# Kernel tuning notes

Hardware: AMD Instinct MI355X
Metric: run time of the kernel (lower is better)

The kernel has to match this reference:

```python
import jax, jax.numpy as jnp
import numpy as np

B = 32768      # number of sets
N = 131072     # total elements
DIM = 128      # feature dim
HID = 64       # hidden dim
MAXP = 17      # max_n + 1 (one-hot positional dim / size-class count)


def _ln(x, g, b, eps=1e-5):
    m = jnp.mean(x, -1, keepdims=True)
    v = jnp.var(x, -1, keepdims=True)
    return (x - m) * jax.lax.rsqrt(v + eps) * g + b


def _mlp_ln(x, w1, b1, g, bt, w2, b2):
    return jnp.tanh(_ln(x @ w1 + b1, g, bt)) @ w2 + b2


def _mlp(x, w1, b1, w2, b2):
    return jnp.tanh(x @ w1 + b1) @ w2 + b2


def _lin_init(key, fan_in, fan_out):
    k1, k2 = jax.random.split(key)
    s = 1.0 / np.sqrt(fan_in)
    return (jax.random.uniform(k1, (fan_in, fan_out), jnp.float32, -s, s),
            jax.random.uniform(k2, (fan_out,), jnp.float32, -s, s))


def setup_inputs() -> dict:
    key = jax.random.key(0)
    ks = jax.random.split(key, 16)
    inp = {}
    inp['x'] = jax.random.normal(ks[0], (N, DIM), jnp.float32)
    inp['batch'] = jnp.sort(jax.random.randint(ks[1], (N,), 0, B)).astype(jnp.int64)
    # rank: Linear(dim, 1)
    inp['rank_w'], inp['rank_b'] = _lin_init(ks[2], DIM, 1)
    # enc_psi: dim -> 96 -> hid, LayerNorm
    inp['psi_w1'], inp['psi_b1'] = _lin_init(ks[3], DIM, 96)
    inp['psi_g'] = jnp.ones((96,), jnp.float32); inp['psi_bt'] = jnp.zeros((96,), jnp.float32)
    inp['psi_w2'], inp['psi_b2'] = _lin_init(ks[4], 96, HID)
    # encoder pos_encoder: 17 -> 40 -> hid, LayerNorm
    inp['pe_e_w1'], inp['pe_e_b1'] = _lin_init(ks[5], MAXP, 40)
    inp['pe_e_g'] = jnp.ones((40,), jnp.float32); inp['pe_e_bt'] = jnp.zeros((40,), jnp.float32)
    inp['pe_e_w2'], inp['pe_e_b2'] = _lin_init(ks[6], 40, HID)
    # enc_phi: (hid+17)=81 -> 72 -> hid, no LN
    inp['phi_w1'], inp['phi_b1'] = _lin_init(ks[7], HID + MAXP, 72)
    inp['phi_w2'], inp['phi_b2'] = _lin_init(ks[8], 72, HID)
    # size_pred: hid -> 40 -> 17, no LN
    inp['size_w1'], inp['size_b1'] = _lin_init(ks[9], HID, 40)
    inp['size_w2'], inp['size_b2'] = _lin_init(ks[10], 40, MAXP)
    # decoder pos_encoder: 17 -> 40 -> hid, LayerNorm
    inp['pe_d_w1'], inp['pe_d_b1'] = _lin_init(ks[11], MAXP, 40)
    inp['pe_d_g'] = jnp.ones((40,), jnp.float32); inp['pe_d_bt'] = jnp.zeros((40,), jnp.float32)
    inp['pe_d_w2'], inp['pe_d_b2'] = _lin_init(ks[12], 40, HID)
    # decoder: hid -> 96 -> dim, no LN
    inp['dec_w1'], inp['dec_b1'] = _lin_init(ks[13], HID, 96)
    inp['dec_w2'], inp['dec_b2'] = _lin_init(ks[14], 96, DIM)
    return inp


def reference(x, batch, rank_w, rank_b,
              psi_w1, psi_b1, psi_g, psi_bt, psi_w2, psi_b2,
              pe_e_w1, pe_e_b1, pe_e_g, pe_e_bt, pe_e_w2, pe_e_b2,
              phi_w1, phi_b1, phi_w2, phi_b2,
              size_w1, size_b1, size_w2, size_b2,
              pe_d_w1, pe_d_b1, pe_d_g, pe_d_bt, pe_d_w2, pe_d_b2,
              dec_w1, dec_b1, dec_w2, dec_b2):
    batch = batch.astype(jnp.int32)
    # ---- Encoder ----
    n = jax.ops.segment_sum(jnp.ones(N, jnp.int32), batch, num_segments=B)  # [B]
    seg_start = jnp.cumsum(n) - n                                           # ptr[:-1]
    mag = (x @ rank_w + rank_b).reshape(-1)                                 # rank scores
    idx = jnp.lexsort((mag, batch))  # per-segment sort (batch is grouped/sorted)
    xs = x[idx]                                                             # [N, DIM]
    keys = jnp.arange(N) - seg_start[batch]                                 # position in set
    pos = jax.nn.one_hot(keys, MAXP, dtype=x.dtype)                         # [N, MAXP]
    y1 = _mlp_ln(xs, psi_w1, psi_b1, psi_g, psi_bt, psi_w2, psi_b2) * \
         _mlp_ln(pos, pe_e_w1, pe_e_b1, pe_e_g, pe_e_bt, pe_e_w2, pe_e_b2)
    y2 = jax.ops.segment_sum(y1, batch, num_segments=B)                     # [B, HID]
    pos_n = jax.nn.one_hot(n, MAXP, dtype=x.dtype)
    z = _mlp(jnp.concatenate([y2, pos_n], -1), phi_w1, phi_b1, phi_w2, phi_b2)  # [B, HID]
    # ---- Decoder ----
    logits = _mlp(z, size_w1, size_b1, size_w2, size_b2)                    # [B, MAXP]
    n_dec = jnp.argmax(logits, -1)                                          # [B]
    pe = _mlp_ln(jnp.eye(MAXP, dtype=x.dtype),
                 pe_d_w1, pe_d_b1, pe_d_g, pe_d_bt, pe_d_w2, pe_d_b2)       # [MAXP, HID]
    zp = z[:, None, :] * pe[None, :, :]                                     # [B, MAXP, HID]
    xr = _mlp(zp, dec_w1, dec_b1, dec_w2, dec_b2)                           # [B, MAXP, DIM]
    mask = jnp.arange(MAXP)[None, :] < n_dec[:, None]                       # valid slots
    xr = jnp.where(mask[..., None], xr, 0.0)
    batchr = jnp.broadcast_to(jnp.arange(B)[:, None], (B, MAXP))
    return xr.reshape(B * MAXP, DIM), batchr.reshape(-1), mask.reshape(-1)
```

## Files before the change

### kernel.cpp

```cpp
#include <hip/hip_runtime.h>

#define NELEM 131072
#define BSETS 32768
#define DIM 128
#define HID 64
#define MAXP 17

typedef __attribute__((ext_vector_type(8))) short short8;
typedef __attribute__((ext_vector_type(4))) float f32x4;

__device__ __forceinline__ unsigned short f2bf(float f) {
  unsigned u = __float_as_uint(f);
  u += 0x7fff + ((u >> 16) & 1);
  return (unsigned short)(u >> 16);
}

__device__ __forceinline__ float fast_tanh(float x) {
  float t = __expf(2.0f * x);
  float r = __builtin_amdgcn_rcpf(t + 1.0f);
  return fmaf(-2.0f, r, 1.0f);
}

__device__ void pos_mlp40(int row, const float* w1, const float* b1, const float* g,
                          const float* bt, const float* w2, const float* b2, float* out) {
  float h[40];
  for (int j = 0; j < 40; ++j) h[j] = b1[j] + (row >= 0 ? w1[row * 40 + j] : 0.0f);
  float s = 0.f;
  for (int j = 0; j < 40; ++j) s += h[j];
  float mean = s * (1.0f / 40.0f);
  float v = 0.f;
  for (int j = 0; j < 40; ++j) { float d = h[j] - mean; v += d * d; }
  float rs = rsqrtf(v * (1.0f / 40.0f) + 1e-5f);
  float tb[40];
  for (int j = 0; j < 40; ++j) tb[j] = fast_tanh((h[j] - mean) * rs * g[j] + bt[j]);
  for (int o = 0; o < 64; ++o) {
    float a = b2[o];
    for (int j = 0; j < 40; ++j) a += tb[j] * w2[j * 64 + o];
    out[o] = a;
  }
}

__global__ __launch_bounds__(256) void k_init(
    const float* __restrict__ x, const int* __restrict__ batch,
    const float* __restrict__ rank_w, const float* __restrict__ rank_b,
    double* __restrict__ mag, int* __restrict__ start,
    const float* ew1, const float* eb1, const float* eg, const float* ebt,
    const float* ew2, const float* eb2,
    const float* dw1, const float* db1, const float* dg, const float* dbt,
    const float* dw2, const float* db2,
    float* enc_tab, float* dec_tab,
    const float* __restrict__ decw1, const float* __restrict__ decw2,
    unsigned short* __restrict__ w1s, unsigned short* __restrict__ w2s) {
  int blk = blockIdx.x;
  int t = threadIdx.x;
  if (blk < 1024) {
    int lane = t & 63;
    int w = t >> 6;
    float2 wv = ((const float2*)rank_w)[lane];
    double w0 = wv.x, w1 = wv.y;
    double rb = rank_b[0];
    int rowbase = (blk * 4 + w) * 32;
    for (int it = 0; it < 32; ++it) {
      int row = rowbase + it;
      float2 xv = ((const float2*)(x + (size_t)row * DIM))[lane];
      double acc = (double)xv.x * w0 + (double)xv.y * w1;
#pragma unroll
      for (int m = 1; m < 64; m <<= 1)
        acc += __shfl_xor(acc, m, 64);
      if (lane == 0) mag[row] = acc + rb;
    }
  } else if (blk < 1536) {
    int i = (blk - 1024) * 256 + t;
    int b = batch[i];
    if (i == 0) {
      for (int bb = 0; bb <= b; ++bb) start[bb] = 0;
    } else {
      int bp = batch[i - 1];
      for (int bb = bp + 1; bb <= b; ++bb) start[bb] = i;
    }
    if (i == NELEM - 1) {
      for (int bb = b + 1; bb <= BSETS; ++bb) start[bb] = NELEM;
    }
  } else if (blk == 1536) {
    if (t < 18) {
      float out[64];
      pos_mlp40(t < 17 ? t : -1, ew1, eb1, eg, ebt, ew2, eb2, out);
      for (int o = 0; o < 64; ++o) enc_tab[t * 64 + o] = out[o];
    } else if (t >= 32 && t < 49) {
      float out[64];
      pos_mlp40(t - 32, dw1, db1, dg, dbt, dw2, db2, out);
      for (int o = 0; o < 64; ++o) dec_tab[(t - 32) * 64 + o] = out[o];
    }
  } else {
    int idx = (blk - 1537) * 256 + t;
    if (idx < 6144) {
      int i = idx & 7, lane = (idx >> 3) & 63, rest = idx >> 9;
      int jt = rest % 6, s = rest / 6;
      int k = s * 32 + (lane >> 4) * 8 + i;
      int n = jt * 16 + (lane & 15);
      w1s[idx] = f2bf(decw1[k * 96 + n]);
    }
    int idx2 = idx - 6144;
    if (idx2 >= 0 && idx2 < 12288) {
      int i = idx2 & 7, lane = (idx2 >> 3) & 63, rest = idx2 >> 9;
      int jt = rest % 8, s = rest / 8;
      int k = s * 32 + (lane >> 4) * 8 + i;
      int n = jt * 16 + (lane & 15);
      w2s[idx2] = f2bf(decw2[k * 128 + n]);
    }
  }
}

__global__ __launch_bounds__(256) void k_encoder(
    const float* __restrict__ x, const int* __restrict__ batch,
    const double* __restrict__ mag, const int* __restrict__ start,
    const float* __restrict__ w1, const float* __restrict__ b1,
    const float* __restrict__ g, const float* __restrict__ bt,
    const float* __restrict__ w2, const float* __restrict__ b2,
    const float* __restrict__ enc_tab, float* __restrict__ y1) {
  __shared__ float sm[64 * 129];
  __shared__ float ps1[4][64];
  __shared__ float ps2[4][64];
  int t = threadIdx.x;
  int base = blockIdx.x * 64;
  const float4* xg = (const float4*)(x + (size_t)base * DIM);
#pragma unroll
  for (int v = 0; v < 8; ++v) {
    int f = t + 256 * v;
    float4 val = xg[f];
    int e = f >> 5, kq = (f & 31) * 4;
    float* xr = sm + e * 129 + kq;
    xr[0] = val.x; xr[1] = val.y; xr[2] = val.z; xr[3] = val.w;
  }
  int lane = t & 63;
  int w = __builtin_amdgcn_readfirstlane(t >> 6);
  int gi = base + lane;
  int bseg = batch[gi];
  int segs = start[bseg], sege = start[bseg + 1];
  double mi = mag[gi];
  int kk = 0;
  for (int j = segs; j < sege; ++j) {
    double mj = mag[j];
    kk += (mj < mi) || (mj == mi && j < gi);
  }
  __syncthreads();
  int j0 = w * 24;
  float acc[24];
#pragma unroll
  for (int jj = 0; jj < 24; ++jj) acc[jj] = b1[j0 + jj];
  for (int k = 0; k < DIM; ++k) {
    float xv = sm[lane * 129 + k];
#pragma unroll
    for (int jj = 0; jj < 24; ++jj) acc[jj] += xv * w1[k * 96 + j0 + jj];
  }
  float s1 = 0.f, s2 = 0.f;
#pragma unroll
  for (int jj = 0; jj < 24; ++jj) { s1 += acc[jj]; s2 += acc[jj] * acc[jj]; }
  ps1[w][lane] = s1; ps2[w][lane] = s2;
  __syncthreads();
  float S1 = ps1[0][lane] + ps1[1][lane] + ps1[2][lane] + ps1[3][lane];
  float S2 = ps2[0][lane] + ps2[1][lane] + ps2[2][lane] + ps2[3][lane];
  float mean = S1 * (1.0f / 96.0f);
  float var = S2 * (1.0f / 96.0f) - mean * mean;
  float rs = rsqrtf(var + 1e-5f);
#pragma unroll
  for (int jj = 0; jj < 24; ++jj) {
    float hv = (acc[jj] - mean) * rs * g[j0 + jj] + bt[j0 + jj];
    sm[lane * 97 + j0 + jj] = fast_tanh(hv);
  }
  __syncthreads();
  int o0 = w * 16;
  float acc2[16];
#pragma unroll
  for (int oo = 0; oo < 16; ++oo) acc2[oo] = b2[o0 + oo];
  for (int j = 0; j < 96; ++j) {
    float tv = sm[lane * 97 + j];
#pragma unroll
    for (int oo = 0; oo < 16; ++oo) acc2[oo] += tv * w2[j * 64 + o0 + oo];
  }
  int row = kk < MAXP ? kk : MAXP;
  int pos = segs + kk;
  const float* pe = enc_tab + row * 64;
#pragma unroll
  for (int oo = 0; oo < 16; ++oo) acc2[oo] *= pe[o0 + oo];
  float4* d4 = (float4*)(y1 + (size_t)pos * 64 + o0);
#pragma unroll
  for (int q = 0; q < 4; ++q)
    d4[q] = make_float4(acc2[4 * q], acc2[4 * q + 1], acc2[4 * q + 2], acc2[4 * q + 3]);
}

__global__ __launch_bounds__(256) void k_phi(const float* __restrict__ y1,
                                             const int* __restrict__ start,
                                             const float* __restrict__ w1, const float* __restrict__ b1,
                                             const float* __restrict__ w2, const float* __restrict__ b2,
                                             const float* __restrict__ sw1, const float* __restrict__ sb1,
                                             const float* __restrict__ sw2, const float* __restrict__ sb2,
                                             float* __restrict__ z, int* __restrict__ ndec) {
  __shared__ float yt[64][65];
  __shared__ float tt[64][73];
  __shared__ float zt[64][65];
  __shared__ float st[64][41];
  int t = threadIdx.x;
  int base = blockIdx.x * 64;
  {
    int s = t >> 2, c = t & 3;
    int sb = base + s;
    int ps = start[sb], pe = start[sb + 1];
    float acc[16];
#pragma unroll
    for (int i = 0; i < 16; ++i) acc[i] = 0.f;
    for (int p = ps; p < pe; ++p) {
      const float4* row = (const float4*)(y1 + (size_t)p * 64 + c * 16);
#pragma unroll
      for (int q = 0; q < 4; ++q) {
        float4 v = row[q];
        acc[4 * q] += v.x; acc[4 * q + 1] += v.y; acc[4 * q + 2] += v.z; acc[4 * q + 3] += v.w;
      }
    }
#pragma unroll
    for (int i = 0; i < 16; ++i) yt[s][c * 16 + i] = acc[i];
  }
  __syncthreads();
  int lane = t & 63;
  int w = __builtin_amdgcn_readfirstlane(t >> 6);
  int sb = base + lane;
  int nb = start[sb + 1] - start[sb];
  int j0 = w * 18;
  float acc[18];
#pragma unroll
  for (int jj = 0; jj < 18; ++jj) acc[jj] = b1[j0 + jj];
  for (int k = 0; k < 64; ++k) {
    float yv = yt[lane][k];
#pragma unroll
    for (int jj = 0; jj < 18; ++jj) acc[jj] += yv * w1[k * 72 + j0 + jj];
  }
  if (nb < MAXP) {
    const float* wr = w1 + (64 + nb) * 72 + j0;
#pragma unroll
    for (int jj = 0; jj < 18; ++jj) acc[jj] += wr[jj];
  }
#pragma unroll
  for (int jj = 0; jj < 18; ++jj) tt[lane][j0 + jj] = fast_tanh(acc[jj]);
  __syncthreads();
  int o0 = w * 16;
  float acc2[16];
#pragma unroll
  for (int oo = 0; oo < 16; ++oo) acc2[oo] = b2[o0 + oo];
  for (int j = 0; j < 72; ++j) {
    float tv = tt[lane][j];
#pragma unroll
    for (int oo = 0; oo < 16; ++oo) acc2[oo] += tv * w2[j * 64 + o0 + oo];
  }
  float4* zd = (float4*)(z + (size_t)sb * 64 + o0);
#pragma unroll
  for (int q = 0; q < 4; ++q)
    zd[q] = make_float4(acc2[4 * q], acc2[4 * q + 1], acc2[4 * q + 2], acc2[4 * q + 3]);
#pragma unroll
  for (int oo = 0; oo < 16; ++oo) zt[lane][o0 + oo] = acc2[oo];
  __syncthreads();
  int s0 = w * 10;
  float hs[10];
#pragma unroll
  for (int jj = 0; jj < 10; ++jj) hs[jj] = sb1[s0 + jj];
  for (int o = 0; o < 64; ++o) {
    float v = zt[lane][o];
#pragma unroll
    for (int jj = 0; jj < 10; ++jj) hs[jj] += v * sw1[o * 40 + s0 + jj];
  }
#pragma unroll
  for (int jj = 0; jj < 10; ++jj) st[lane][s0 + jj] = fast_tanh(hs[jj]);
  __syncthreads();
  if (w == 0) {
    float lg[17];
#pragma unroll
    for (int l = 0; l < 17; ++l) lg[l] = sb2[l];
    for (int j = 0; j < 40; ++j) {
      float tv = st[lane][j];
#pragma unroll
      for (int l = 0; l < 17; ++l) lg[l] += tv * sw2[j * 17 + l];
    }
    float best = lg[0]; int bi = 0;
#pragma unroll
    for (int l = 1; l < 17; ++l) if (lg[l] > best) { best = lg[l]; bi = l; }
    ndec[sb] = bi;
  }
}

__global__ __launch_bounds__(256) void k_decoder(
    const float* __restrict__ z, const float* __restrict__ dec_tab,
    const unsigned short* __restrict__ w1s, const unsigned short* __restrict__ w2s,
    const float* __restrict__ b1, const float* __restrict__ b2,
    const int* __restrict__ ndec, float* __restrict__ out0,
    float* __restrict__ out1, float* __restrict__ out2) {
  __shared__ __align__(16) unsigned short h2[64][104];
  int t = threadIdx.x;
  int lane = t & 63;
  int w = __builtin_amdgcn_readfirstlane(t >> 6);
  int quad = lane >> 4, m = lane & 15;
  int r = blockIdx.x * 64 + w * 16 + m;
  int b = r / 17, p = r - b * 17;
  const float4* z4 = (const float4*)(z + (size_t)b * 64);
  const float4* p4 = (const float4*)(dec_tab + p * 64);
  short8 a1[2];
#pragma unroll
  for (int s = 0; s < 2; ++s) {
    int q0 = (s * 32 + quad * 8) >> 2;
    float4 za = z4[q0], zb = z4[q0 + 1];
    float4 pa = p4[q0], pb = p4[q0 + 1];
    unsigned short* ap = (unsigned short*)&a1[s];
    ap[0] = f2bf(za.x * pa.x); ap[1] = f2bf(za.y * pa.y);
    ap[2] = f2bf(za.z * pa.z); ap[3] = f2bf(za.w * pa.w);
    ap[4] = f2bf(zb.x * pb.x); ap[5] = f2bf(zb.y * pb.y);
    ap[6] = f2bf(zb.z * pb.z); ap[7] = f2bf(zb.w * pb.w);
  }
  const short8* w1f = (const short8*)w1s;
  f32x4 acc[6] = {};
#pragma unroll
  for (int jt = 0; jt < 6; ++jt) {
    acc[jt] = __builtin_amdgcn_mfma_f32_16x16x32_bf16(a1[0], w1f[jt * 64 + lane], acc[jt], 0, 0, 0);
    acc[jt] = __builtin_amdgcn_mfma_f32_16x16x32_bf16(a1[1], w1f[(6 + jt) * 64 + lane], acc[jt], 0, 0, 0);
  }
#pragma unroll
  for (int jt = 0; jt < 6; ++jt) {
    int col = jt * 16 + m;
    float bias = b1[col];
#pragma unroll
    for (int reg = 0; reg < 4; ++reg) {
      int rl = w * 16 + quad * 4 + reg;
      h2[rl][col] = f2bf(fast_tanh(acc[jt][reg] + bias));
    }
  }
  __syncthreads();
  short8 a2[3];
#pragma unroll
  for (int s = 0; s < 3; ++s)
    a2[s] = *(const short8*)&h2[w * 16 + m][s * 32 + quad * 8];
  const short8* w2f = (const short8*)w2s;
  f32x4 acc2[8] = {};
#pragma unroll
  for (int nt = 0; nt < 8; ++nt) {
#pragma unroll
    for (int s = 0; s < 3; ++s)
      acc2[nt] = __builtin_amdgcn_mfma_f32_16x16x32_bf16(a2[s], w2f[(s * 8 + nt) * 64 + lane], acc2[nt], 0, 0, 0);
  }
#pragma unroll
  for (int nt = 0; nt < 8; ++nt) {
    int n = nt * 16 + m;
    float bias = b2[n];
#pragma unroll
    for (int reg = 0; reg < 4; ++reg) {
      int rl = w * 16 + quad * 4 + reg;
      int rg = blockIdx.x * 64 + rl;
      int bb = rg / 17, pp = rg - bb * 17;
      float v = acc2[nt][reg] + bias;
      if (pp >= ndec[bb]) v = 0.0f;
      out0[(size_t)rg * 128 + n] = v;
    }
  }
  if (t < 64) {
    int rg = blockIdx.x * 64 + t;
    int bb = rg / 17, pp = rg - bb * 17;
    out1[rg] = (float)bb;
    out2[rg] = (pp < ndec[bb]) ? 1.0f : 0.0f;
  }
}

extern "C" void kernel_launch(void* const* d_in, const int* in_sizes, int n_in,
                              void* d_out, int out_size, void* d_ws, size_t ws_size,
                              hipStream_t stream) {
  const float* x = (const float*)d_in[0];
  const int* batch = (const int*)d_in[1];
  const float* rank_w = (const float*)d_in[2];
  const float* rank_b = (const float*)d_in[3];
  const float* psi_w1 = (const float*)d_in[4];
  const float* psi_b1 = (const float*)d_in[5];
  const float* psi_g = (const float*)d_in[6];
  const float* psi_bt = (const float*)d_in[7];
  const float* psi_w2 = (const float*)d_in[8];
  const float* psi_b2 = (const float*)d_in[9];
  const float* pe_e_w1 = (const float*)d_in[10];
  const float* pe_e_b1 = (const float*)d_in[11];
  const float* pe_e_g = (const float*)d_in[12];
  const float* pe_e_bt = (const float*)d_in[13];
  const float* pe_e_w2 = (const float*)d_in[14];
  const float* pe_e_b2 = (const float*)d_in[15];
  const float* phi_w1 = (const float*)d_in[16];
  const float* phi_b1 = (const float*)d_in[17];
  const float* phi_w2 = (const float*)d_in[18];
  const float* phi_b2 = (const float*)d_in[19];
  const float* size_w1 = (const float*)d_in[20];
  const float* size_b1 = (const float*)d_in[21];
  const float* size_w2 = (const float*)d_in[22];
  const float* size_b2 = (const float*)d_in[23];
  const float* pe_d_w1 = (const float*)d_in[24];
  const float* pe_d_b1 = (const float*)d_in[25];
  const float* pe_d_g = (const float*)d_in[26];
  const float* pe_d_bt = (const float*)d_in[27];
  const float* pe_d_w2 = (const float*)d_in[28];
  const float* pe_d_b2 = (const float*)d_in[29];
  const float* dec_w1 = (const float*)d_in[30];
  const float* dec_b1 = (const float*)d_in[31];
  const float* dec_w2 = (const float*)d_in[32];
  const float* dec_b2 = (const float*)d_in[33];

  char* ws = (char*)d_ws;
  int* start = (int*)(ws);
  double* mag = (double*)(ws + 0x40000);
  float* enc_tab = (float*)(ws + 0x1C0000);
  float* dec_tab = (float*)(ws + 0x1C2000);
  unsigned short* w1s = (unsigned short*)(ws + 0x1C4000);
  unsigned short* w2s = (unsigned short*)(ws + 0x1C8000);
  float* zbuf = (float*)(ws + 0x200000);
  int* ndec = (int*)(ws + 0xA00000);

  float* out0 = (float*)d_out;
  float* out1 = out0 + 71303168;
  float* out2 = out1 + 557056;

  float* y1 = out0;

  k_init<<<1609, 256, 0, stream>>>(x, batch, rank_w, rank_b, mag, start,
                                   pe_e_w1, pe_e_b1, pe_e_g, pe_e_bt, pe_e_w2, pe_e_b2,
                                   pe_d_w1, pe_d_b1, pe_d_g, pe_d_bt, pe_d_w2, pe_d_b2,
                                   enc_tab, dec_tab, dec_w1, dec_w2, w1s, w2s);
  k_encoder<<<2048, 256, 0, stream>>>(x, batch, mag, start, psi_w1, psi_b1, psi_g, psi_bt,
                                      psi_w2, psi_b2, enc_tab, y1);
  k_phi<<<512, 256, 0, stream>>>(y1, start, phi_w1, phi_b1, phi_w2, phi_b2,
                                 size_w1, size_b1, size_w2, size_b2, zbuf, ndec);
  k_decoder<<<8704, 256, 0, stream>>>(zbuf, dec_tab, w1s, w2s, dec_b1, dec_b2, ndec,
                                      out0, out1, out2);
}
```

Before: 627.1 us.

## Move encoder psi MLP to split-bf16 MFMA with pre-swizzled hi/lo weights

Replaces the scalar FP32 FMA loops of the encoder's psi MLP with bf16 MFMA 16x16x32 instructions. Weights are split into high and low bf16 parts (three-term products) and pre-swizzled in k_init to keep near-fp32 accuracy. LayerNorm statistics are now reduced with cross-lane shuffles instead of shared-memory partials, and the rank computation runs on one wave. The decoder's per-row mask computation is hoisted out of the column loop. This adds a prep phase and triples MFMA work in exchange for removing scalar FMA throughput limits.

```diff
diff --git a/kernel.cpp b/kernel.cpp
--- a/kernel.cpp
+++ b/kernel.cpp
@@ -13,6 +13,10 @@
   unsigned u = __float_as_uint(f);
   u += 0x7fff + ((u >> 16) & 1);
   return (unsigned short)(u >> 16);
+}
+
+__device__ __forceinline__ float bf2f(unsigned short h) {
+  return __uint_as_float((unsigned)h << 16);
 }
 
 __device__ __forceinline__ float fast_tanh(float x) {
@@ -50,7 +54,10 @@
     const float* dw2, const float* db2,
     float* enc_tab, float* dec_tab,
     const float* __restrict__ decw1, const float* __restrict__ decw2,
-    unsigned short* __restrict__ w1s, unsigned short* __restrict__ w2s) {
+    unsigned short* __restrict__ w1s, unsigned short* __restrict__ w2s,
+    const float* __restrict__ psiw1, const float* __restrict__ psiw2,
+    unsigned short* __restrict__ pw1h, unsigned short* __restrict__ pw1l,
+    unsigned short* __restrict__ pw2h, unsigned short* __restrict__ pw2l) {
   int blk = blockIdx.x;
   int t = threadIdx.x;
   if (blk < 1024) {
@@ -108,85 +115,168 @@
       int n = jt * 16 + (lane & 15);
       w2s[idx2] = f2bf(decw2[k * 128 + n]);
     }
+    int idx3 = idx - 18432;
+    if (idx3 >= 0 && idx3 < 12288) {
+      int i = idx3 & 7, lane = (idx3 >> 3) & 63, rest = idx3 >> 9;
+      int jt = rest % 6, s = rest / 6;
+      int k = s * 32 + (lane >> 4) * 8 + i;
+      int n = jt * 16 + (lane & 15);
+      float v = psiw1[k * 96 + n];
+      unsigned short h = f2bf(v);
+      pw1h[idx3] = h;
+      pw1l[idx3] = f2bf(v - bf2f(h));
+    }
+    int idx4 = idx - 30720;
+    if (idx4 >= 0 && idx4 < 6144) {
+      int i = idx4 & 7, lane = (idx4 >> 3) & 63, rest = idx4 >> 9;
+      int nt = rest % 4, s = rest / 4;
+      int k = s * 32 + (lane >> 4) * 8 + i;
+      int n = nt * 16 + (lane & 15);
+      float v = psiw2[k * 64 + n];
+      unsigned short h = f2bf(v);
+      pw2h[idx4] = h;
+      pw2l[idx4] = f2bf(v - bf2f(h));
+    }
   }
 }
 
 __global__ __launch_bounds__(256) void k_encoder(
     const float* __restrict__ x, const int* __restrict__ batch,
     const double* __restrict__ mag, const int* __restrict__ start,
-    const float* __restrict__ w1, const float* __restrict__ b1,
-    const float* __restrict__ g, const float* __restrict__ bt,
-    const float* __restrict__ w2, const float* __restrict__ b2,
+    const unsigned short* __restrict__ w1h, const unsigned short* __restrict__ w1l,
+    const float* __restrict__ b1, const float* __restrict__ g, const float* __restrict__ bt,
+    const unsigned short* __restrict__ w2h, const unsigned short* __restrict__ w2l,
+    const float* __restrict__ b2,
     const float* __restrict__ enc_tab, float* __restrict__ y1) {
-  __shared__ float sm[64 * 129];
-  __shared__ float ps1[4][64];
-  __shared__ float ps2[4][64];
+  __shared__ float tt[64][100];
+  __shared__ int pos_s[64];
+  __shared__ int row_s[64];
   int t = threadIdx.x;
-  int base = blockIdx.x * 64;
-  const float4* xg = (const float4*)(x + (size_t)base * DIM);
-#pragma unroll
-  for (int v = 0; v < 8; ++v) {
-    int f = t + 256 * v;
-    float4 val = xg[f];
-    int e = f >> 5, kq = (f & 31) * 4;
-    float* xr = sm + e * 129 + kq;
-    xr[0] = val.x; xr[1] = val.y; xr[2] = val.z; xr[3] = val.w;
-  }
   int lane = t & 63;
   int w = __builtin_amdgcn_readfirstlane(t >> 6);
-  int gi = base + lane;
-  int bseg = batch[gi];
-  int segs = start[bseg], sege = start[bseg + 1];
-  double mi = mag[gi];
-  int kk = 0;
-  for (int j = segs; j < sege; ++j) {
-    double mj = mag[j];
-    kk += (mj < mi) || (mj == mi && j < gi);
+  int base = blockIdx.x * 64;
+  int r = lane & 15, gq = lane >> 4;
+
+  if (w == 0) {
+    int gi = base + lane;
+    int b = batch[gi];
+    int segs = start[b], sege = start[b + 1];
+    double mi = mag[gi];
+    int kk = 0;
+    for (int j = segs; j < sege; ++j) {
+      double mj = mag[j];
+      kk += (mj < mi) || (mj == mi && j < gi);
+    }
+    pos_s[lane] = segs + kk;
+    row_s[lane] = kk < MAXP ? kk : MAXP;
+  }
+
+  const float* xr = x + (size_t)(base + w * 16 + r) * DIM + gq * 8;
+  short8 ah[4], al[4];
+#pragma unroll
+  for (int s = 0; s < 4; ++s) {
+    float4 v0 = *(const float4*)(xr + s * 32);
+    float4 v1 = *(const float4*)(xr + s * 32 + 4);
+    float vv[8] = {v0.x, v0.y, v0.z, v0.w, v1.x, v1.y, v1.z, v1.w};
+#pragma unroll
+    for (int i = 0; i < 8; ++i) {
+      unsigned short h = f2bf(vv[i]);
+      ((unsigned short*)&ah[s])[i] = h;
+      ((unsigned short*)&al[s])[i] = f2bf(vv[i] - bf2f(h));
+    }
+  }
+
+  const short8* W1H = (const short8*)w1h;
+  const short8* W1L = (const short8*)w1l;
+  f32x4 acc1[6] = {};
+#pragma unroll
+  for (int jt = 0; jt < 6; ++jt) {
+#pragma unroll
+    for (int s = 0; s < 4; ++s) {
+      short8 bh = W1H[(s * 6 + jt) * 64 + lane];
+      short8 bl = W1L[(s * 6 + jt) * 64 + lane];
+      acc1[jt] = __builtin_amdgcn_mfma_f32_16x16x32_bf16(ah[s], bh, acc1[jt], 0, 0, 0);
+      acc1[jt] = __builtin_amdgcn_mfma_f32_16x16x32_bf16(ah[s], bl, acc1[jt], 0, 0, 0);
+      acc1[jt] = __builtin_amdgcn_mfma_f32_16x16x32_bf16(al[s], bh, acc1[jt], 0, 0, 0);
+    }
+  }
+
+  float b1v[6], gv[6], btv[6];
+#pragma unroll
+  for (int jt = 0; jt < 6; ++jt) {
+    b1v[jt] = b1[jt * 16 + r];
+    gv[jt] = g[jt * 16 + r];
+    btv[jt] = bt[jt * 16 + r];
+  }
+#pragma unroll
+  for (int reg = 0; reg < 4; ++reg) {
+    float h[6];
+    float s1 = 0.f, s2 = 0.f;
+#pragma unroll
+    for (int jt = 0; jt < 6; ++jt) {
+      h[jt] = acc1[jt][reg] + b1v[jt];
+      s1 += h[jt]; s2 += h[jt] * h[jt];
+    }
+#pragma unroll
+    for (int m = 1; m < 16; m <<= 1) {
+      s1 += __shfl_xor(s1, m, 64);
+      s2 += __shfl_xor(s2, m, 64);
+    }
+    float mean = s1 * (1.0f / 96.0f);
+    float var = s2 * (1.0f / 96.0f) - mean * mean;
+    float rs = rsqrtf(var + 1e-5f);
+    int rowl = w * 16 + gq * 4 + reg;
+#pragma unroll
+    for (int jt = 0; jt < 6; ++jt)
+      tt[rowl][jt * 16 + r] = fast_tanh((h[jt] - mean) * rs * gv[jt] + btv[jt]);
   }
   __syncthreads();
-  int j0 = w * 24;
-  float acc[24];
-#pragma unroll
-  for (int jj = 0; jj < 24; ++jj) acc[jj] = b1[j0 + jj];
-  for (int k = 0; k < DIM; ++k) {
-    float xv = sm[lane * 129 + k];
-#pragma unroll
-    for (int jj = 0; jj < 24; ++jj) acc[jj] += xv * w1[k * 96 + j0 + jj];
-  }
-  float s1 = 0.f, s2 = 0.f;
-#pragma unroll
-  for (int jj = 0; jj < 24; ++jj) { s1 += acc[jj]; s2 += acc[jj] * acc[jj]; }
-  ps1[w][lane] = s1; ps2[w][lane] = s2;
-  __syncthreads();
-  float S1 = ps1[0][lane] + ps1[1][lane] + ps1[2][lane] + ps1[3][lane];
-  float S2 = ps2[0][lane] + ps2[1][lane] + ps2[2][lane] + ps2[3][lane];
-  float mean = S1 * (1.0f / 96.0f);
-  float var = S2 * (1.0f / 96.0f) - mean * mean;
-  float rs = rsqrtf(var + 1e-5f);
-#pragma unroll
-  for (int jj = 0; jj < 24; ++jj) {
-    float hv = (acc[jj] - mean) * rs * g[j0 + jj] + bt[j0 + jj];
-    sm[lane * 97 + j0 + jj] = fast_tanh(hv);
-  }
-  __syncthreads();
-  int o0 = w * 16;
-  float acc2[16];
-#pragma unroll
-  for (int oo = 0; oo < 16; ++oo) acc2[oo] = b2[o0 + oo];
-  for (int j = 0; j < 96; ++j) {
-    float tv = sm[lane * 97 + j];
-#pragma unroll
-    for (int oo = 0; oo < 16; ++oo) acc2[oo] += tv * w2[j * 64 + o0 + oo];
-  }
-  int row = kk < MAXP ? kk : MAXP;
-  int pos = segs + kk;
-  const float* pe = enc_tab + row * 64;
-#pragma unroll
-  for (int oo = 0; oo < 16; ++oo) acc2[oo] *= pe[o0 + oo];
-  float4* d4 = (float4*)(y1 + (size_t)pos * 64 + o0);
-#pragma unroll
-  for (int q = 0; q < 4; ++q)
-    d4[q] = make_float4(acc2[4 * q], acc2[4 * q + 1], acc2[4 * q + 2], acc2[4 * q + 3]);
+
+  const float* trow = &tt[w * 16 + r][0] + gq * 8;
+  short8 a2h[3], a2l[3];
+#pragma unroll
+  for (int s = 0; s < 3; ++s) {
+    float4 u0 = *(const float4*)(trow + s * 32);
+    float4 u1 = *(const float4*)(trow + s * 32 + 4);
+    float vv[8] = {u0.x, u0.y, u0.z, u0.w, u1.x, u1.y, u1.z, u1.w};
+#pragma unroll
+    for (int i = 0; i < 8; ++i) {
+      unsigned short h = f2bf(vv[i]);
+      ((unsigned short*)&a2h[s])[i] = h;
+      ((unsigned short*)&a2l[s])[i] = f2bf(vv[i] - bf2f(h));
+    }
+  }
+
+  const short8* W2H = (const short8*)w2h;
+  const short8* W2L = (const short8*)w2l;
+  f32x4 acc2[4] = {};
+#pragma unroll
+  for (int nt = 0; nt < 4; ++nt) {
+#pragma unroll
+    for (int s = 0; s < 3; ++s) {
+      short8 bh = W2H[(s * 4 + nt) * 64 + lane];
+      short8 bl = W2L[(s * 4 + nt) * 64 + lane];
+      acc2[nt] = __builtin_amdgcn_mfma_f32_16x16x32_bf16(a2h[s], bh, acc2[nt], 0, 0, 0);
+      acc2[nt] = __builtin_amdgcn_mfma_f32_16x16x32_bf16(a2h[s], bl, acc2[nt], 0, 0, 0);
+      acc2[nt] = __builtin_amdgcn_mfma_f32_16x16x32_bf16(a2l[s], bh, acc2[nt], 0, 0, 0);
+    }
+  }
+
+  float b2v[4];
+#pragma unroll
+  for (int nt = 0; nt < 4; ++nt) b2v[nt] = b2[nt * 16 + r];
+#pragma unroll
+  for (int reg = 0; reg < 4; ++reg) {
+    int rowl = w * 16 + gq * 4 + reg;
+    int pos = pos_s[rowl];
+    const float* pe = enc_tab + row_s[rowl] * 64;
+    float* yd = y1 + (size_t)pos * 64;
+#pragma unroll
+    for (int nt = 0; nt < 4; ++nt) {
+      int col = nt * 16 + r;
+      yd[col] = (acc2[nt][reg] + b2v[nt]) * pe[col];
+    }
+  }
 }
 
 __global__ __launch_bounds__(256) void k_phi(const float* __restrict__ y1,
@@ -343,18 +433,23 @@
     for (int s = 0; s < 3; ++s)
       acc2[nt] = __builtin_amdgcn_mfma_f32_16x16x32_bf16(a2[s], w2f[(s * 8 + nt) * 64 + lane], acc2[nt], 0, 0, 0);
   }
+  int rgbase = blockIdx.x * 64 + w * 16 + quad * 4;
+  bool mk[4];
+#pragma unroll
+  for (int reg = 0; reg < 4; ++reg) {
+    int rg = rgbase + reg;
+    int bb = rg / 17, pp = rg - bb * 17;
+    mk[reg] = (pp >= ndec[bb]);
+  }
 #pragma unroll
   for (int nt = 0; nt < 8; ++nt) {
     int n = nt * 16 + m;
     float bias = b2[n];
 #pragma unroll
     for (int reg = 0; reg < 4; ++reg) {
-      int rl = w * 16 + quad * 4 + reg;
-      int rg = blockIdx.x * 64 + rl;
-      int bb = rg / 17, pp = rg - bb * 17;
       float v = acc2[nt][reg] + bias;
-      if (pp >= ndec[bb]) v = 0.0f;
-      out0[(size_t)rg * 128 + n] = v;
+      if (mk[reg]) v = 0.0f;
+      out0[(size_t)(rgbase + reg) * 128 + n] = v;
     }
   }
   if (t < 64) {
@@ -410,6 +505,10 @@
   float* dec_tab = (float*)(ws + 0x1C2000);
   unsigned short* w1s = (unsigned short*)(ws + 0x1C4000);
   unsigned short* w2s = (unsigned short*)(ws + 0x1C8000);
+  unsigned short* pw1h = (unsigned short*)(ws + 0x1CE000);
+  unsigned short* pw1l = (unsigned short*)(ws + 0x1D4000);
+  unsigned short* pw2h = (unsigned short*)(ws + 0x1DA000);
+  unsigned short* pw2l = (unsigned short*)(ws + 0x1DD000);
   float* zbuf = (float*)(ws + 0x200000);
   int* ndec = (int*)(ws + 0xA00000);
 
@@ -419,12 +518,14 @@
 
   float* y1 = out0;
 
-  k_init<<<1609, 256, 0, stream>>>(x, batch, rank_w, rank_b, mag, start,
+  k_init<<<1681, 256, 0, stream>>>(x, batch, rank_w, rank_b, mag, start,
                                    pe_e_w1, pe_e_b1, pe_e_g, pe_e_bt, pe_e_w2, pe_e_b2,
                                    pe_d_w1, pe_d_b1, pe_d_g, pe_d_bt, pe_d_w2, pe_d_b2,
-                                   enc_tab, dec_tab, dec_w1, dec_w2, w1s, w2s);
-  k_encoder<<<2048, 256, 0, stream>>>(x, batch, mag, start, psi_w1, psi_b1, psi_g, psi_bt,
-                                      psi_w2, psi_b2, enc_tab, y1);
+                                   enc_tab, dec_tab, dec_w1, dec_w2, w1s, w2s,
+                                   psi_w1, psi_w2, pw1h, pw1l, pw2h, pw2l);
+  k_encoder<<<2048, 256, 0, stream>>>(x, batch, mag, start, pw1h, pw1l,
+                                      psi_b1, psi_g, psi_bt, pw2h, pw2l, psi_b2,
+                                      enc_tab, y1);
   k_phi<<<512, 256, 0, stream>>>(y1, start, phi_w1, phi_b1, phi_w2, phi_b2,
                                  size_w1, size_b1, size_w2, size_b2, zbuf, ndec);
   k_decoder<<<8704, 256, 0, stream>>>(zbuf, dec_tab, w1s, w2s, dec_b1, dec_b2, ndec,
```

Measured after the change: 570.8 us. 1.1x faster.
